# Performance work log

Measured on AMD Instinct MI355X. Metric: run time of the kernel, lower is better.

## Reference

```python
import jax, jax.numpy as jnp
import numpy as np

B, T, C, R = 4, 2048, 2048, 256


def setup_inputs() -> dict:
    key = jax.random.key(0)
    ks = jax.random.split(key, 12)
    s = 0.02
    return {
        "x": jax.random.normal(ks[0], (B, T, C), dtype=jnp.float32),
        "h_state": jnp.zeros((B, C), dtype=jnp.float32),
        "ln_gamma": jnp.ones((C,), dtype=jnp.float32),
        "ln_beta": jnp.zeros((C,), dtype=jnp.float32),
        "wq_a": jax.random.normal(ks[1], (C, R), dtype=jnp.float32) * s,
        "wq_b": jax.random.normal(ks[2], (R, C), dtype=jnp.float32) * s,
        "wk_a": jax.random.normal(ks[3], (C, R), dtype=jnp.float32) * s,
        "wk_b": jax.random.normal(ks[4], (R, C), dtype=jnp.float32) * s,
        "wv_a": jax.random.normal(ks[5], (C, R), dtype=jnp.float32) * s,
        "wv_b": jax.random.normal(ks[6], (R, C), dtype=jnp.float32) * s,
        "out_w": jax.random.normal(ks[7], (C, C), dtype=jnp.float32) * s,
        "out_b": jnp.zeros((C,), dtype=jnp.float32),
        "time_decay": jnp.full((C,), -0.5, dtype=jnp.float32),
    }


def _layernorm(x, gamma, beta, eps=1e-5):
    mu = jnp.mean(x, axis=-1, keepdims=True)
    var = jnp.var(x, axis=-1, keepdims=True)
    return (x - mu) * jax.lax.rsqrt(var + eps) * gamma + beta


def reference(x, h_state, ln_gamma, ln_beta, wq_a, wq_b, wk_a, wk_b, wv_a, wv_b, out_w, out_b, time_decay):
    b, t, c = x.shape
    xn = _layernorm(x, ln_gamma, ln_beta)
    # token shift: mix current with previous token
    x_shift = jnp.concatenate([jnp.zeros((b, 1, c), xn.dtype), xn[:, :-1, :]], axis=1)
    mix = 0.5 * xn + 0.5 * x_shift
    # low-rank projections: (B,T,C) @ (C,R) @ (R,C)
    q = jnp.einsum('btc,cr,rd->btd', mix, wq_a, wq_b)
    k = jnp.einsum('btc,cr,rd->btd', mix, wk_a, wk_b)
    v = jnp.einsum('btc,cr,rd->btd', mix, wv_a, wv_b)
    decay = jnp.exp(-jnp.exp(time_decay))  # (C,)

    kv = (k * v).transpose(1, 0, 2)          # (T,B,C)
    sq = jax.nn.sigmoid(q).transpose(1, 0, 2)  # (T,B,C)

    def step(h, inp):
        kv_t, sq_t = inp
        h = decay * h + kv_t
        return h, sq_t * h

    h_final, ys = jax.lax.scan(step, h_state, (kv, sq))
    out = ys.transpose(1, 0, 2)               # (B,T,C)
    out = jnp.einsum('btc,dc->btd', out, out_w) + out_b
    return out, h_final
```

## Files before the change

### kernel.cpp

```cpp
#include <hip/hip_runtime.h>


typedef __attribute__((ext_vector_type(8))) __bf16 bf16x8;
typedef __attribute__((ext_vector_type(4))) float f32x4;

static constexpr int Bb = 4, Tt = 2048, Cc = 2048, Rr = 256;
static constexpr int Mrows = Bb * Tt;
static constexpr int NCH = 32, CLEN = 64;

__device__ __forceinline__ unsigned short f2bf(float f) {
  union { float f; unsigned u; } a; a.f = f;
  unsigned r = (a.u + 0x7FFFu + ((a.u >> 16) & 1u)) >> 16;
  return (unsigned short)r;
}
__device__ __forceinline__ float bf2f(unsigned short h) {
  union { unsigned u; float f; } a; a.u = ((unsigned)h) << 16;
  return a.f;
}

__device__ __forceinline__ void gload16(const void* g, void* l) {
  __builtin_amdgcn_global_load_lds(
      (const __attribute__((address_space(1))) void*)g,
      (__attribute__((address_space(3))) void*)l, 16, 0, 0);
}

__global__ void prep_weights(const float* __restrict__ wqa, const float* __restrict__ wka,
                             const float* __restrict__ wva, const float* __restrict__ wqb,
                             const float* __restrict__ wkb, const float* __restrict__ wvb,
                             const float* __restrict__ ow,  const float* __restrict__ td,
                             unsigned short* __restrict__ waT, unsigned short* __restrict__ wbT,
                             unsigned short* __restrict__ owT, float* __restrict__ decay,
                             float* __restrict__ decayL) {
  const int g = blockIdx.x * blockDim.x + threadIdx.x;
  const int stride = gridDim.x * blockDim.x;
  for (int i = g; i < 3 * Rr * Cc; i += stride) {
    int c = i & (Cc - 1); int jj = i >> 11; int p = jj >> 8; int r = jj & (Rr - 1);
    const float* w = (p == 0) ? wqa : ((p == 1) ? wka : wva);
    waT[i] = f2bf(w[(size_t)c * Rr + r]);
  }
  for (int i = g; i < 3 * Cc * Rr; i += stride) {
    int r = i & (Rr - 1); int d = (i >> 8) & (Cc - 1); int p = i >> 19;
    const float* w = (p == 0) ? wqb : ((p == 1) ? wkb : wvb);
    wbT[i] = f2bf(w[(size_t)r * Cc + d]);
  }
  for (int i = g; i < Cc * Cc; i += stride) owT[i] = f2bf(ow[i]);
  for (int i = g; i < Cc; i += stride) {
    float e = expf(td[i]);
    decay[i] = expf(-e);
    decayL[i] = expf(-(float)CLEN * e);
  }
}

__global__ void ln_stats_kernel(const float* __restrict__ x, float* __restrict__ stats) {
  const int row = blockIdx.x;
  const float* xr = x + (size_t)row * Cc;
  float sum = 0.f, sq = 0.f;
  for (int i = threadIdx.x; i < Cc / 4; i += 256) {
    float4 v = ((const float4*)xr)[i];
    sum += v.x + v.y + v.z + v.w;
    sq  += v.x * v.x + v.y * v.y + v.z * v.z + v.w * v.w;
  }
  for (int off = 32; off; off >>= 1) {
    sum += __shfl_down(sum, off);
    sq  += __shfl_down(sq, off);
  }
  __shared__ float s[8];
  if ((threadIdx.x & 63) == 0) { s[(threadIdx.x >> 6) * 2] = sum; s[(threadIdx.x >> 6) * 2 + 1] = sq; }
  __syncthreads();
  if (threadIdx.x == 0) {
    float ts = 0.f, tq = 0.f;
    for (int wv = 0; wv < 4; ++wv) { ts += s[wv * 2]; tq += s[wv * 2 + 1]; }
    float mean = ts * (1.0f / Cc);
    float var  = tq * (1.0f / Cc) - mean * mean;
    stats[row * 2] = mean;
    stats[row * 2 + 1] = rsqrtf(var + 1e-5f);
  }
}

__global__ void mix_kernel(const float* __restrict__ x, const float* __restrict__ stats,
                           const float* __restrict__ gamma, const float* __restrict__ beta,
                           unsigned short* __restrict__ mix) {
  const int total4 = Mrows * (Cc / 4);
  for (int i = blockIdx.x * blockDim.x + threadIdx.x; i < total4; i += gridDim.x * blockDim.x) {
    const int c4 = i & (Cc / 4 - 1);
    const int m  = i >> 9;
    const int t  = m & (Tt - 1);
    const float4 xv = ((const float4*)x)[i];
    const float mu = stats[2 * m], rs = stats[2 * m + 1];
    const float4 g  = ((const float4*)gamma)[c4];
    const float4 bb = ((const float4*)beta)[c4];
    float mx = (xv.x - mu) * rs * g.x + bb.x;
    float my = (xv.y - mu) * rs * g.y + bb.y;
    float mz = (xv.z - mu) * rs * g.z + bb.z;
    float mw = (xv.w - mu) * rs * g.w + bb.w;
    if (t > 0) {
      const float4 pv = ((const float4*)x)[i - Cc / 4];
      const float pmu = stats[2 * (m - 1)], prs = stats[2 * (m - 1) + 1];
      mx = 0.5f * (mx + (pv.x - pmu) * prs * g.x + bb.x);
      my = 0.5f * (my + (pv.y - pmu) * prs * g.y + bb.y);
      mz = 0.5f * (mz + (pv.z - pmu) * prs * g.z + bb.z);
      mw = 0.5f * (mw + (pv.w - pmu) * prs * g.w + bb.w);
    } else {
      mx *= 0.5f; my *= 0.5f; mz *= 0.5f; mw *= 0.5f;
    }
    ushort4 o;
    o.x = f2bf(mx); o.y = f2bf(my); o.z = f2bf(mz); o.w = f2bf(mw);
    ((ushort4*)mix)[i] = o;
  }
}

template <bool STORE_BF16, bool ADD_BIAS>
__global__ __launch_bounds__(512, 2) void gemm_pipe(
    const unsigned short* __restrict__ A0p, long lda, long aStrideP,
    const unsigned short* __restrict__ B0p, long ldb, long bStrideP,
    void* c0, void* c1, void* c2, long ldc, int K,
    const float* __restrict__ bias, int nbx, int nby) {
  __shared__ unsigned short lds[4 * 16384];
  const int tid = threadIdx.x;
  const int nwg = gridDim.x;
  const int id = blockIdx.x;
  const int q = nwg >> 3;
  const int swz = (id & 7) * q + (id >> 3);
  const int per = nbx * nby;
  const int p = swz / per;
  const int r2 = swz - p * per;
  const int mblk = r2 / nbx;
  const int nblk = r2 - mblk * nbx;
  const unsigned short* A  = A0p + (long)p * aStrideP;
  const unsigned short* Bt = B0p + (long)p * bStrideP;
  void* Cout = (p == 0) ? c0 : (p == 1 ? c1 : c2);
  const long m0 = (long)mblk * 256, n0 = (long)nblk * 256;

  const int lane = tid & 63, wid = tid >> 6;
  const int wm = wid >> 2, wn = wid & 3;
  const int fr = lane & 15, fq = lane >> 4;

  const int srow = tid >> 2;
  const int s_src = (tid & 3) ^ ((tid >> 3) & 3);
  const unsigned short* Ag = A + (m0 + srow) * lda + s_src * 8;
  const unsigned short* Bg = Bt + (n0 + srow) * ldb + s_src * 8;

  const int swzs = fq ^ ((fr >> 1) & 3);
  const unsigned short* aBase = &lds[(wm * 128 + fr) * 32 + swzs * 8];
  const unsigned short* bBase = &lds[8192 + (wn * 64 + fr) * 32 + swzs * 8];

  f32x4 acc[8][4];
#pragma unroll
  for (int i = 0; i < 8; ++i)
#pragma unroll
    for (int j = 0; j < 4; ++j) acc[i][j] = (f32x4){0.f, 0.f, 0.f, 0.f};

  const int NT = K >> 5;

  auto stageA = [&](int t) {
    unsigned short* d = &lds[(t & 3) * 16384 + tid * 8];
    const long kt = (long)t * 32;
    gload16(Ag + kt, d);
    gload16(Ag + 128 * lda + kt, d + 4096);
  };
  auto stageB = [&](int t) {
    unsigned short* d = &lds[(t & 3) * 16384 + 8192 + tid * 8];
    const long kt = (long)t * 32;
    gload16(Bg + kt, d);
    gload16(Bg + 128 * ldb + kt, d + 4096);
  };

  stageA(0); stageB(0);
  stageA(1); stageB(1);
  stageA(2); stageB(2);

  for (int t = 0; t < NT; ++t) {
    const int rem = NT - 1 - t;
    if (rem >= 2)      asm volatile("s_waitcnt vmcnt(8)" ::: "memory");
    else if (rem == 1) asm volatile("s_waitcnt vmcnt(4)" ::: "memory");
    else               asm volatile("s_waitcnt vmcnt(0)" ::: "memory");
    __builtin_amdgcn_s_barrier();

    const unsigned short* ab = aBase + (t & 3) * 16384;
    const unsigned short* bb = bBase + (t & 3) * 16384;

    bf16x8 bf[4];
#pragma unroll
    for (int j = 0; j < 4; ++j) bf[j] = *(const bf16x8*)(bb + j * 512);
    bf16x8 af[4];
#pragma unroll
    for (int i = 0; i < 4; ++i) af[i] = *(const bf16x8*)(ab + i * 512);
    if (t + 3 < NT) stageA(t + 3);
    __builtin_amdgcn_s_barrier();
    __builtin_amdgcn_s_setprio(1);
#pragma unroll
    for (int i = 0; i < 4; ++i)
#pragma unroll
      for (int j = 0; j < 4; ++j)
        acc[i][j] = __builtin_amdgcn_mfma_f32_16x16x32_bf16(af[i], bf[j], acc[i][j], 0, 0, 0);
    __builtin_amdgcn_s_setprio(0);
    __builtin_amdgcn_s_barrier();

#pragma unroll
    for (int i = 0; i < 4; ++i) af[i] = *(const bf16x8*)(ab + (4 + i) * 512);
    if (t + 3 < NT) stageB(t + 3);
    __builtin_amdgcn_s_barrier();
    __builtin_amdgcn_s_setprio(1);
#pragma unroll
    for (int i = 0; i < 4; ++i)
#pragma unroll
      for (int j = 0; j < 4; ++j)
        acc[4 + i][j] = __builtin_amdgcn_mfma_f32_16x16x32_bf16(af[i], bf[j], acc[4 + i][j], 0, 0, 0);
    __builtin_amdgcn_s_setprio(0);
  }

#pragma unroll
  for (int j = 0; j < 4; ++j) {
    const long col = n0 + wn * 64 + j * 16 + fr;
    const float bv = ADD_BIAS ? bias[col] : 0.0f;
#pragma unroll
    for (int i = 0; i < 8; ++i) {
      const long row0 = m0 + wm * 128 + i * 16 + fq * 4;
#pragma unroll
      for (int r = 0; r < 4; ++r) {
        float val = acc[i][j][r] + bv;
        if (STORE_BF16)
          ((unsigned short*)Cout)[(row0 + r) * ldc + col] = f2bf(val);
        else
          ((float*)Cout)[(row0 + r) * ldc + col] = val;
      }
    }
  }
}

__global__ void scan_phaseA(const unsigned short* __restrict__ k, const unsigned short* __restrict__ v,
                            const float* __restrict__ decay, float* __restrict__ hend) {
  const int g = blockIdx.x * 256 + threadIdx.x;
  const int c = g & (Cc - 1);
  const int j = (g >> 11) & (NCH - 1);
  const int b = g >> 16;
  const float d = decay[c];
  size_t base = ((size_t)(b * Tt + j * CLEN)) * Cc + c;
  float h = 0.f;
#pragma unroll 8
  for (int s = 0; s < CLEN; ++s) {
    size_t idx = base + (size_t)s * Cc;
    float kv = bf2f(k[idx]) * bf2f(v[idx]);
    h = fmaf(d, h, kv);
  }
  hend[(size_t)(b * NCH + j) * Cc + c] = h;
}

__global__ void scan_combine(const float* __restrict__ hend, const float* __restrict__ h0,
                             const float* __restrict__ decayL, float* __restrict__ Hin,
                             float* __restrict__ hfinal) {
  const int g = blockIdx.x * 256 + threadIdx.x;
  const int c = g & (Cc - 1);
  float H = h0[g];
  const float dl = decayL[c];
  const int b = g >> 11;
  for (int j = 0; j < NCH; ++j) {
    size_t idx = (size_t)(b * NCH + j) * Cc + c;
    Hin[idx] = H;
    H = fmaf(dl, H, hend[idx]);
  }
  hfinal[g] = H;
}

__global__ void scan_phaseB(const unsigned short* __restrict__ q, const unsigned short* __restrict__ k,
                            const unsigned short* __restrict__ v, const float* __restrict__ decay,
                            const float* __restrict__ Hin, unsigned short* __restrict__ ys) {
  const int g = blockIdx.x * 256 + threadIdx.x;
  const int c = g & (Cc - 1);
  const int j = (g >> 11) & (NCH - 1);
  const int b = g >> 16;
  const float d = decay[c];
  float h = Hin[(size_t)(b * NCH + j) * Cc + c];
  size_t base = ((size_t)(b * Tt + j * CLEN)) * Cc + c;
#pragma unroll 4
  for (int s = 0; s < CLEN; ++s) {
    size_t idx = base + (size_t)s * Cc;
    float kv = bf2f(k[idx]) * bf2f(v[idx]);
    h = fmaf(d, h, kv);
    float qq = bf2f(q[idx]);
    float sg = 1.f / (1.f + expf(-qq));
    ys[idx] = f2bf(sg * h);
  }
}

extern "C" void kernel_launch(void* const* d_in, const int* in_sizes, int n_in,
                              void* d_out, int out_size, void* d_ws, size_t ws_size,
                              hipStream_t stream) {
  const float* x   = (const float*)d_in[0];
  const float* h0  = (const float*)d_in[1];
  const float* gam = (const float*)d_in[2];
  const float* bet = (const float*)d_in[3];
  const float* wqa = (const float*)d_in[4];
  const float* wqb = (const float*)d_in[5];
  const float* wka = (const float*)d_in[6];
  const float* wkb = (const float*)d_in[7];
  const float* wva = (const float*)d_in[8];
  const float* wvb = (const float*)d_in[9];
  const float* ow  = (const float*)d_in[10];
  const float* ob  = (const float*)d_in[11];
  const float* td  = (const float*)d_in[12];
  float* out = (float*)d_out;

  char* ws = (char*)d_ws;
  unsigned short* waT   = (unsigned short*)(ws + 0);
  unsigned short* wbT   = (unsigned short*)(ws + 3145728);
  unsigned short* owT   = (unsigned short*)(ws + 6291456);
  float*          decay = (float*)(ws + 14680064);
  float*          decayL= (float*)(ws + 14688256);
  float*          stats = (float*)(ws + 14696448);
  unsigned short* mixb  = (unsigned short*)(ws + 14761984);
  unsigned short* tmp   = (unsigned short*)(ws + 48316416);
  unsigned short* vp    = (unsigned short*)(ws + 60899328);
  float*          hend  = (float*)(ws + 94453760);
  float*          Hin   = (float*)(ws + 95502336);
  unsigned short* qp = (unsigned short*)d_out;
  unsigned short* kp = qp + (size_t)Mrows * Cc;
  float* hfinal = out + (size_t)Mrows * Cc;
  unsigned short* ysb = mixb;

  prep_weights<<<1024, 256, 0, stream>>>(wqa, wka, wva, wqb, wkb, wvb, ow, td,
                                         waT, wbT, owT, decay, decayL);
  ln_stats_kernel<<<Mrows, 256, 0, stream>>>(x, stats);
  mix_kernel<<<2048, 256, 0, stream>>>(x, stats, gam, bet, mixb);

  gemm_pipe<true, false><<<96, 512, 0, stream>>>(
      mixb, Cc, 0, waT, Cc, 0,
      tmp, tmp, tmp, 768, Cc, nullptr, 3, 32);

  gemm_pipe<true, false><<<8 * 32 * 3, 512, 0, stream>>>(
      tmp, 768, 256, wbT, Rr, (long)Cc * Rr,
      qp, kp, vp, Cc, Rr, nullptr, 8, 32);

  scan_phaseA<<<(Bb * NCH * Cc) / 256, 256, 0, stream>>>(kp, vp, decay, hend);
  scan_combine<<<(Bb * Cc) / 256, 256, 0, stream>>>(hend, h0, decayL, Hin, hfinal);
  scan_phaseB<<<(Bb * NCH * Cc) / 256, 256, 0, stream>>>(qp, kp, vp, decay, Hin, ysb);

  gemm_pipe<false, true><<<8 * 32, 512, 0, stream>>>(
      ysb, Cc, 0, owT, Cc, 0,
      out, out, out, Cc, Cc, ob, 8, 32);
}
```

Baseline: 280.5 us.

## Fuse layernorm into mix, split-K first projection, merge GEMM loop phases

Merges the layernorm statistics and token-shift mix into one per-row kernel that recomputes the previous row's statistics, so the stats buffer and a second pass over x go away. The first low-rank GEMM, which launched only 96 workgroups, now splits K into two halves, writing fp32 partials into the output buffer, and a new add-and-convert kernel sums them into bf16. The GEMM main loop now loads all A fragments at once and issues both stage loads together, dropping the intermediate barriers to cut synchronisation. The costs are extra fp32 partial traffic, one more launch, and higher register pressure from holding eight A fragments.

```diff
diff --git a/kernel.cpp b/kernel.cpp
--- a/kernel.cpp
+++ b/kernel.cpp
@@ -51,61 +51,77 @@
   }
 }
 
-__global__ void ln_stats_kernel(const float* __restrict__ x, float* __restrict__ stats) {
-  const int row = blockIdx.x;
-  const float* xr = x + (size_t)row * Cc;
-  float sum = 0.f, sq = 0.f;
-  for (int i = threadIdx.x; i < Cc / 4; i += 256) {
+__global__ __launch_bounds__(256) void lnmix_kernel(
+    const float* __restrict__ x, const float* __restrict__ gamma,
+    const float* __restrict__ beta, unsigned short* __restrict__ mix) {
+  const int m = blockIdx.x;
+  const int t = m & (Tt - 1);
+  const float* xr = x + (size_t)m * Cc;
+  float s0 = 0.f, q0 = 0.f, s1 = 0.f, q1 = 0.f;
+  float4 cur[2], prv[2];
+#pragma unroll
+  for (int r = 0; r < 2; ++r) {
+    int i = threadIdx.x + r * 256;
     float4 v = ((const float4*)xr)[i];
-    sum += v.x + v.y + v.z + v.w;
-    sq  += v.x * v.x + v.y * v.y + v.z * v.z + v.w * v.w;
-  }
+    cur[r] = v;
+    s0 += v.x + v.y + v.z + v.w;
+    q0 += v.x * v.x + v.y * v.y + v.z * v.z + v.w * v.w;
+  }
+  if (t > 0) {
+    const float* xp = xr - Cc;
+#pragma unroll
+    for (int r = 0; r < 2; ++r) {
+      int i = threadIdx.x + r * 256;
+      float4 v = ((const float4*)xp)[i];
+      prv[r] = v;
+      s1 += v.x + v.y + v.z + v.w;
+      q1 += v.x * v.x + v.y * v.y + v.z * v.z + v.w * v.w;
+    }
+  }
+#pragma unroll
   for (int off = 32; off; off >>= 1) {
-    sum += __shfl_down(sum, off);
-    sq  += __shfl_down(sq, off);
-  }
-  __shared__ float s[8];
-  if ((threadIdx.x & 63) == 0) { s[(threadIdx.x >> 6) * 2] = sum; s[(threadIdx.x >> 6) * 2 + 1] = sq; }
+    s0 += __shfl_down(s0, off); q0 += __shfl_down(q0, off);
+    s1 += __shfl_down(s1, off); q1 += __shfl_down(q1, off);
+  }
+  __shared__ float red[4][4];
+  __shared__ float bc[4];
+  if ((threadIdx.x & 63) == 0) {
+    int w = threadIdx.x >> 6;
+    red[w][0] = s0; red[w][1] = q0; red[w][2] = s1; red[w][3] = q1;
+  }
   __syncthreads();
   if (threadIdx.x == 0) {
-    float ts = 0.f, tq = 0.f;
-    for (int wv = 0; wv < 4; ++wv) { ts += s[wv * 2]; tq += s[wv * 2 + 1]; }
-    float mean = ts * (1.0f / Cc);
-    float var  = tq * (1.0f / Cc) - mean * mean;
-    stats[row * 2] = mean;
-    stats[row * 2 + 1] = rsqrtf(var + 1e-5f);
-  }
-}
-
-__global__ void mix_kernel(const float* __restrict__ x, const float* __restrict__ stats,
-                           const float* __restrict__ gamma, const float* __restrict__ beta,
-                           unsigned short* __restrict__ mix) {
-  const int total4 = Mrows * (Cc / 4);
-  for (int i = blockIdx.x * blockDim.x + threadIdx.x; i < total4; i += gridDim.x * blockDim.x) {
-    const int c4 = i & (Cc / 4 - 1);
-    const int m  = i >> 9;
-    const int t  = m & (Tt - 1);
-    const float4 xv = ((const float4*)x)[i];
-    const float mu = stats[2 * m], rs = stats[2 * m + 1];
-    const float4 g  = ((const float4*)gamma)[c4];
-    const float4 bb = ((const float4*)beta)[c4];
-    float mx = (xv.x - mu) * rs * g.x + bb.x;
-    float my = (xv.y - mu) * rs * g.y + bb.y;
-    float mz = (xv.z - mu) * rs * g.z + bb.z;
-    float mw = (xv.w - mu) * rs * g.w + bb.w;
+    float a0 = 0, b0 = 0, a1 = 0, b1 = 0;
+    for (int w = 0; w < 4; ++w) { a0 += red[w][0]; b0 += red[w][1]; a1 += red[w][2]; b1 += red[w][3]; }
+    float mu0 = a0 * (1.f / Cc);
+    bc[0] = mu0; bc[1] = rsqrtf(b0 * (1.f / Cc) - mu0 * mu0 + 1e-5f);
+    float mu1 = a1 * (1.f / Cc);
+    bc[2] = mu1; bc[3] = rsqrtf(b1 * (1.f / Cc) - mu1 * mu1 + 1e-5f);
+  }
+  __syncthreads();
+  const float mu0 = bc[0], rs0 = bc[1], mu1 = bc[2], rs1 = bc[3];
+#pragma unroll
+  for (int r = 0; r < 2; ++r) {
+    int i = threadIdx.x + r * 256;
+    float4 g = ((const float4*)gamma)[i];
+    float4 bb = ((const float4*)beta)[i];
+    float4 v = cur[r];
+    float mx = (v.x - mu0) * rs0 * g.x + bb.x;
+    float my = (v.y - mu0) * rs0 * g.y + bb.y;
+    float mz = (v.z - mu0) * rs0 * g.z + bb.z;
+    float mw = (v.w - mu0) * rs0 * g.w + bb.w;
     if (t > 0) {
-      const float4 pv = ((const float4*)x)[i - Cc / 4];
-      const float pmu = stats[2 * (m - 1)], prs = stats[2 * (m - 1) + 1];
-      mx = 0.5f * (mx + (pv.x - pmu) * prs * g.x + bb.x);
-      my = 0.5f * (my + (pv.y - pmu) * prs * g.y + bb.y);
-      mz = 0.5f * (mz + (pv.z - pmu) * prs * g.z + bb.z);
-      mw = 0.5f * (mw + (pv.w - pmu) * prs * g.w + bb.w);
+      float4 u = prv[r];
+      mx = 0.5f * (mx + (u.x - mu1) * rs1 * g.x + bb.x);
+      my = 0.5f * (my + (u.y - mu1) * rs1 * g.y + bb.y);
+      mz = 0.5f * (mz + (u.z - mu1) * rs1 * g.z + bb.z);
+      mw = 0.5f * (mw + (u.w - mu1) * rs1 * g.w + bb.w);
     } else {
       mx *= 0.5f; my *= 0.5f; mz *= 0.5f; mw *= 0.5f;
     }
     ushort4 o;
     o.x = f2bf(mx); o.y = f2bf(my); o.z = f2bf(mz); o.w = f2bf(mw);
-    ((ushort4*)mix)[i] = o;
+    ((ushort4*)mix)[(size_t)m * 512 + i] = o;
   }
 }
 
@@ -175,37 +191,23 @@
     else if (rem == 1) asm volatile("s_waitcnt vmcnt(4)" ::: "memory");
     else               asm volatile("s_waitcnt vmcnt(0)" ::: "memory");
     __builtin_amdgcn_s_barrier();
+    __builtin_amdgcn_sched_barrier(0);
 
     const unsigned short* ab = aBase + (t & 3) * 16384;
     const unsigned short* bb = bBase + (t & 3) * 16384;
 
-    bf16x8 bf[4];
+    bf16x8 bf[4], af[8];
 #pragma unroll
     for (int j = 0; j < 4; ++j) bf[j] = *(const bf16x8*)(bb + j * 512);
-    bf16x8 af[4];
-#pragma unroll
-    for (int i = 0; i < 4; ++i) af[i] = *(const bf16x8*)(ab + i * 512);
-    if (t + 3 < NT) stageA(t + 3);
-    __builtin_amdgcn_s_barrier();
+#pragma unroll
+    for (int i = 0; i < 8; ++i) af[i] = *(const bf16x8*)(ab + i * 512);
+    if (t + 3 < NT) { stageA(t + 3); stageB(t + 3); }
     __builtin_amdgcn_s_setprio(1);
 #pragma unroll
-    for (int i = 0; i < 4; ++i)
+    for (int i = 0; i < 8; ++i)
 #pragma unroll
       for (int j = 0; j < 4; ++j)
         acc[i][j] = __builtin_amdgcn_mfma_f32_16x16x32_bf16(af[i], bf[j], acc[i][j], 0, 0, 0);
-    __builtin_amdgcn_s_setprio(0);
-    __builtin_amdgcn_s_barrier();
-
-#pragma unroll
-    for (int i = 0; i < 4; ++i) af[i] = *(const bf16x8*)(ab + (4 + i) * 512);
-    if (t + 3 < NT) stageB(t + 3);
-    __builtin_amdgcn_s_barrier();
-    __builtin_amdgcn_s_setprio(1);
-#pragma unroll
-    for (int i = 0; i < 4; ++i)
-#pragma unroll
-      for (int j = 0; j < 4; ++j)
-        acc[4 + i][j] = __builtin_amdgcn_mfma_f32_16x16x32_bf16(af[i], bf[j], acc[4 + i][j], 0, 0, 0);
     __builtin_amdgcn_s_setprio(0);
   }
 
@@ -225,6 +227,18 @@
           ((float*)Cout)[(row0 + r) * ldc + col] = val;
       }
     }
+  }
+}
+
+__global__ void addcvt_kernel(const float* __restrict__ p0, const float* __restrict__ p1,
+                              unsigned short* __restrict__ o, int n4) {
+  for (int i = blockIdx.x * blockDim.x + threadIdx.x; i < n4; i += gridDim.x * blockDim.x) {
+    float4 a = ((const float4*)p0)[i];
+    float4 b = ((const float4*)p1)[i];
+    ushort4 r;
+    r.x = f2bf(a.x + b.x); r.y = f2bf(a.y + b.y);
+    r.z = f2bf(a.z + b.z); r.w = f2bf(a.w + b.w);
+    ((ushort4*)o)[i] = r;
   }
 }
 
@@ -307,12 +321,13 @@
   unsigned short* owT   = (unsigned short*)(ws + 6291456);
   float*          decay = (float*)(ws + 14680064);
   float*          decayL= (float*)(ws + 14688256);
-  float*          stats = (float*)(ws + 14696448);
   unsigned short* mixb  = (unsigned short*)(ws + 14761984);
   unsigned short* tmp   = (unsigned short*)(ws + 48316416);
   unsigned short* vp    = (unsigned short*)(ws + 60899328);
   float*          hend  = (float*)(ws + 94453760);
   float*          Hin   = (float*)(ws + 95502336);
+  float* P0 = (float*)d_out;
+  float* P1 = P0 + (size_t)Mrows * 768;
   unsigned short* qp = (unsigned short*)d_out;
   unsigned short* kp = qp + (size_t)Mrows * Cc;
   float* hfinal = out + (size_t)Mrows * Cc;
@@ -320,12 +335,12 @@
 
   prep_weights<<<1024, 256, 0, stream>>>(wqa, wka, wva, wqb, wkb, wvb, ow, td,
                                          waT, wbT, owT, decay, decayL);
-  ln_stats_kernel<<<Mrows, 256, 0, stream>>>(x, stats);
-  mix_kernel<<<2048, 256, 0, stream>>>(x, stats, gam, bet, mixb);
-
-  gemm_pipe<true, false><<<96, 512, 0, stream>>>(
-      mixb, Cc, 0, waT, Cc, 0,
-      tmp, tmp, tmp, 768, Cc, nullptr, 3, 32);
+  lnmix_kernel<<<Mrows, 256, 0, stream>>>(x, gam, bet, mixb);
+
+  gemm_pipe<false, false><<<192, 512, 0, stream>>>(
+      mixb, Cc, 1024, waT, Cc, 1024,
+      P0, P1, nullptr, 768, 1024, nullptr, 3, 32);
+  addcvt_kernel<<<1024, 256, 0, stream>>>(P0, P1, tmp, Mrows * 768 / 4);
 
   gemm_pipe<true, false><<<8 * 32 * 3, 512, 0, stream>>>(
       tmp, 768, 256, wbT, Rr, (long)Cc * Rr,
```

New measurement: 255.2 us. -9.0%, faster.
